# Kernel optimization log

Measured on AMD Instinct MI355X. Metric: run time of the kernel, lower is better.

The kernel has to match this reference:

```python
import jax, jax.numpy as jnp
import numpy as np

NUM_HEADS = 16
ROPE_THETA = 10000.0


def apply_rope(x, positions):
    # x: [B, H, S, D], positions: [S] int
    d = x.shape[-1]
    inv_freq = ROPE_THETA ** (-jnp.arange(0, d, 2, dtype=jnp.float32) / d)  # [D/2]
    ang = positions.astype(jnp.float32)[:, None] * inv_freq[None, :]        # [S, D/2]
    cos, sin = jnp.cos(ang), jnp.sin(ang)                                   # [S, D/2]
    x1, x2 = x[..., 0::2], x[..., 1::2]                                     # even/odd pairs
    r1 = x1 * cos - x2 * sin
    r2 = x1 * sin + x2 * cos
    return jnp.stack([r1, r2], axis=-1).reshape(x.shape)


def setup_inputs() -> dict:
    key = jax.random.key(0)
    k1, k2, k3 = jax.random.split(key, 3)
    B, S, D = 2, 2048, 2048
    x = jax.random.normal(k1, (B, S, D), dtype=jnp.float32)
    token_positions = jnp.arange(S, dtype=jnp.int64)
    w_qkv = jax.random.normal(k2, (D, 3 * D), dtype=jnp.float32) * (D ** -0.5)
    w_o = jax.random.normal(k3, (D, D), dtype=jnp.float32) * (D ** -0.5)
    return {"x": x, "token_positions": token_positions, "w_qkv": w_qkv, "w_o": w_o}


def reference(x, token_positions, w_qkv, w_o):
    B, S, D = x.shape
    H = NUM_HEADS
    hd = D // H
    qkv = x @ w_qkv                                   # [B, S, 3D]
    qkv = qkv.reshape(B, S, 3, H, hd)                 # split '(r h d)'
    q = jnp.transpose(qkv[:, :, 0], (0, 2, 1, 3))     # [B, H, S, hd]
    k = jnp.transpose(qkv[:, :, 1], (0, 2, 1, 3))
    v = jnp.transpose(qkv[:, :, 2], (0, 2, 1, 3))
    q = apply_rope(q, token_positions)
    k = apply_rope(k, token_positions)
    scale = 1.0 / jnp.sqrt(jnp.float32(hd))
    scores = jnp.einsum('bhqd,bhkd->bhqk', q, k) * scale  # [B, H, S, S]
    causal = jnp.tril(jnp.ones((S, S), dtype=bool))
    scores = jnp.where(causal[None, None], scores, jnp.float32(-1e30))
    attn = jax.nn.softmax(scores, axis=-1)
    a = jnp.einsum('bhqk,bhkd->bhqd', attn, v)            # [B, H, S, hd]
    a = jnp.transpose(a, (0, 2, 1, 3)).reshape(B, S, D)   # merge heads, h-major
    return a @ w_o
```

## Files before the change

### kernel.cpp

```cpp
#include <hip/hip_runtime.h>

#define SEQ  2048
#define DIM  2048
#define NH   16
#define HD   128
#define TDIM 6144
#define TT   4096

typedef float  f32x4  __attribute__((ext_vector_type(4)));
typedef __bf16 bf16x8 __attribute__((ext_vector_type(8)));

__device__ __forceinline__ unsigned short f2b(float f){
  union { float f; unsigned int u; } x; x.f = f;
  unsigned int r = x.u + 0x7FFFu + ((x.u >> 16) & 1u);
  return (unsigned short)(r >> 16);
}
__device__ __forceinline__ float b2f(unsigned short b){
  union { unsigned int u; float f; } x; x.u = ((unsigned int)b) << 16;
  return x.f;
}
__device__ __forceinline__ void gl_lds16(const void* g, void* l){
  __builtin_amdgcn_global_load_lds((const __attribute__((address_space(1))) unsigned int*)g,
                                   (__attribute__((address_space(3))) unsigned int*)l, 16, 0, 0);
}

__global__ __launch_bounds__(256) void k_prep(const float* __restrict__ x,
                                              unsigned short* __restrict__ xb,
                                              float2* __restrict__ tab){
  int bid = blockIdx.x;
  if (bid < 8192){
    int i = bid * 256 + threadIdx.x;
    float4 v = ((const float4*)x)[i];
    ushort4 o; o.x = f2b(v.x); o.y = f2b(v.y); o.z = f2b(v.z); o.w = f2b(v.w);
    ((ushort4*)xb)[i] = o;
  } else {
    int i = (bid - 8192) * 256 + threadIdx.x;
    int s = i >> 6, f = i & 63;
    double inv = pow(10000.0, -2.0 * (double)f / 128.0);
    double a = (double)s * inv;
    tab[i] = make_float2((float)cos(a), (float)sin(a));
  }
}

__global__ __launch_bounds__(256) void k_tconvB(const float* __restrict__ w_qkv,
                                                unsigned short* __restrict__ wqkvT,
                                                const float* __restrict__ w_o,
                                                unsigned short* __restrict__ woT){
  const float* in; unsigned short* out; int C;
  if (blockIdx.z == 0){ in = w_qkv; out = wqkvT; C = TDIM; }
  else                { in = w_o;   out = woT;   C = DIM;  }
  int c0 = blockIdx.x * 32;
  if (c0 >= C) return;
  __shared__ float t[64][33];
  int r0 = blockIdx.y * 64;
  int tx = threadIdx.x & 31, ty = threadIdx.x >> 5;
  for (int i = 0; i < 8; i++)
    t[ty + i*8][tx] = in[(size_t)(r0 + ty + i*8) * C + c0 + tx];
  __syncthreads();
  for (int i = 0; i < 4; i++){
    int c = ty + i*8;
    ushort2 o2; o2.x = f2b(t[2*tx][c]); o2.y = f2b(t[2*tx+1][c]);
    *(ushort2*)&out[(size_t)(c0 + c) * DIM + r0 + 2*tx] = o2;
  }
}

__global__ __launch_bounds__(256) void k_tv(const unsigned short* __restrict__ qkv,
                                            unsigned short* __restrict__ vT){
  __shared__ unsigned short t[64][65];
  int bh = blockIdx.z; int b = bh >> 4, h = bh & 15;
  const unsigned short* V = qkv + (size_t)b * SEQ * TDIM + 2 * DIM + h * HD;
  unsigned short* o = vT + (size_t)bh * HD * SEQ;
  int s0 = blockIdx.x * 64, d0 = blockIdx.y * 64;
  int tx = threadIdx.x & 31, ty = threadIdx.x >> 5;
  for (int i = 0; i < 8; i++){
    unsigned int v = *(const unsigned int*)&V[(size_t)(s0 + ty + i*8) * TDIM + d0 + 2*tx];
    t[ty + i*8][2*tx]   = (unsigned short)(v & 0xffffu);
    t[ty + i*8][2*tx+1] = (unsigned short)(v >> 16);
  }
  __syncthreads();
  for (int i = 0; i < 8; i++){
    int d = ty + i*8;
    ushort2 o2; o2.x = t[2*tx][d]; o2.y = t[2*tx+1][d];
    *(ushort2*)&o[(size_t)(d0 + d) * SEQ + s0 + 2*tx] = o2;
  }
}

template<bool OUT_F32, bool ROPE>
__global__ __launch_bounds__(512, 2) void k_gemm2(const unsigned short* __restrict__ A,
                                                  const unsigned short* __restrict__ BT,
                                                  void* __restrict__ Cout,
                                                  int M, int N, int K,
                                                  const float2* __restrict__ tab){
  __shared__ unsigned short sA[2*2*8192];
  __shared__ unsigned short sB[2*2*8192];
  int tid = threadIdx.x;
  int w = tid >> 6, l = tid & 63;
  int lm = l & 15, lq = l >> 4;
  int wm = w >> 2, wn = w & 3;
  int m0 = blockIdx.y * 256, n0 = blockIdx.x * 256;
  int NT = K >> 6;

  auto stA = [&](int buf, int half, int u){
    unsigned short* dst = sA + (buf*2 + half) * 8192;
    int grow0 = m0 + half*128;
#pragma unroll
    for (int j2 = 0; j2 < 2; j2++){
      int g = j2*512 + tid;
      int r = g >> 3, gc = g & 7;
      gl_lds16(A + (size_t)(grow0 + r) * K + u*64 + ((gc ^ (r & 7)) * 8), dst + g*8);
    }
  };
  auto stB = [&](int buf, int half, int u){
    unsigned short* dst = sB + (buf*2 + half) * 8192;
    int grow0 = n0 + half*128;
#pragma unroll
    for (int j2 = 0; j2 < 2; j2++){
      int g = j2*512 + tid;
      int r = g >> 3, gc = g & 7;
      gl_lds16(BT + (size_t)(grow0 + r) * K + u*64 + ((gc ^ (r & 7)) * 8), dst + g*8);
    }
  };

  f32x4 acc[2][2][4][2] = {};

  stA(0, 0, 0); stB(0, 1, 0); stA(0, 1, 0); stB(0, 0, 0);
  stA(1, 0, 1); stB(1, 1, 1);
  asm volatile("s_waitcnt vmcnt(4)" ::: "memory");
  __builtin_amdgcn_s_barrier();

  for (int t = 0; t < NT; t++){
    int cur = t & 1, nb = cur ^ 1;
    const unsigned short* sAb = sA + cur * 16384;
    const unsigned short* sBb = sB + cur * 16384;
    bf16x8 a[4][2], b0[2][2], b1[2][2];

#pragma unroll
    for (int i = 0; i < 4; i++){
      int r = wm*64 + i*16 + lm;
#pragma unroll
      for (int s = 0; s < 2; s++)
        a[i][s] = *(const bf16x8*)&sAb[r*64 + (((s*4 + lq) ^ (r & 7)) * 8)];
    }
#pragma unroll
    for (int j = 0; j < 2; j++){
      int r = wn*32 + j*16 + lm;
#pragma unroll
      for (int s = 0; s < 2; s++)
        b0[j][s] = *(const bf16x8*)&sBb[r*64 + (((s*4 + lq) ^ (r & 7)) * 8)];
    }
    __builtin_amdgcn_sched_barrier(0);
#pragma unroll
    for (int j = 0; j < 2; j++){
      int r = wn*32 + j*16 + lm;
#pragma unroll
      for (int s = 0; s < 2; s++)
        b1[j][s] = *(const bf16x8*)&sBb[8192 + r*64 + (((s*4 + lq) ^ (r & 7)) * 8)];
    }
    if (t + 1 < NT) stA(nb, 1, t + 1);
    asm volatile("s_waitcnt lgkmcnt(4)" ::: "memory");
    __builtin_amdgcn_sched_barrier(0);
    __builtin_amdgcn_s_setprio(1);
#pragma unroll
    for (int s = 0; s < 2; s++)
#pragma unroll
      for (int i = 0; i < 4; i++)
#pragma unroll
        for (int j = 0; j < 2; j++)
          acc[0][0][i][j] = __builtin_amdgcn_mfma_f32_16x16x32_bf16(a[i][s], b0[j][s],
                                                                    acc[0][0][i][j], 0, 0, 0);
    __builtin_amdgcn_s_setprio(0);
    __builtin_amdgcn_s_barrier();

    if (t + 1 < NT) stB(nb, 0, t + 1);
    asm volatile("s_waitcnt lgkmcnt(0)" ::: "memory");
    __builtin_amdgcn_sched_barrier(0);
    __builtin_amdgcn_s_setprio(1);
#pragma unroll
    for (int s = 0; s < 2; s++)
#pragma unroll
      for (int i = 0; i < 4; i++)
#pragma unroll
        for (int j = 0; j < 2; j++)
          acc[0][1][i][j] = __builtin_amdgcn_mfma_f32_16x16x32_bf16(a[i][s], b1[j][s],
                                                                    acc[0][1][i][j], 0, 0, 0);
    __builtin_amdgcn_s_setprio(0);
    __builtin_amdgcn_sched_barrier(0);
#pragma unroll
    for (int i = 0; i < 4; i++){
      int r = wm*64 + i*16 + lm;
#pragma unroll
      for (int s = 0; s < 2; s++)
        a[i][s] = *(const bf16x8*)&sAb[8192 + r*64 + (((s*4 + lq) ^ (r & 7)) * 8)];
    }
    __builtin_amdgcn_s_barrier();

    if (t + 2 < NT) stA(cur, 0, t + 2);
    asm volatile("s_waitcnt lgkmcnt(0)" ::: "memory");
    __builtin_amdgcn_sched_barrier(0);
    __builtin_amdgcn_s_setprio(1);
#pragma unroll
    for (int s = 0; s < 2; s++)
#pragma unroll
      for (int i = 0; i < 4; i++)
#pragma unroll
        for (int j = 0; j < 2; j++)
          acc[1][1][i][j] = __builtin_amdgcn_mfma_f32_16x16x32_bf16(a[i][s], b1[j][s],
                                                                    acc[1][1][i][j], 0, 0, 0);
    __builtin_amdgcn_s_setprio(0);
    __builtin_amdgcn_s_barrier();

    if (t + 2 < NT) stB(cur, 1, t + 2);
    __builtin_amdgcn_s_setprio(1);
#pragma unroll
    for (int s = 0; s < 2; s++)
#pragma unroll
      for (int i = 0; i < 4; i++)
#pragma unroll
        for (int j = 0; j < 2; j++)
          acc[1][0][i][j] = __builtin_amdgcn_mfma_f32_16x16x32_bf16(a[i][s], b0[j][s],
                                                                    acc[1][0][i][j], 0, 0, 0);
    __builtin_amdgcn_s_setprio(0);
    if (t + 2 < NT) asm volatile("s_waitcnt vmcnt(4)" ::: "memory");
    else            asm volatile("s_waitcnt vmcnt(0)" ::: "memory");
    __builtin_amdgcn_s_barrier();
  }

#pragma unroll
  for (int qm = 0; qm < 2; qm++)
#pragma unroll
    for (int qn = 0; qn < 2; qn++)
#pragma unroll
      for (int i = 0; i < 4; i++)
#pragma unroll
        for (int j = 0; j < 2; j++)
#pragma unroll
          for (int r = 0; r < 4; r++){
            int row = m0 + qm*128 + wm*64 + i*16 + lq*4 + r;
            int col = n0 + qn*128 + wn*32 + j*16 + lm;
            float v = acc[qm][qn][i][j][r];
            if (ROPE && col < 2*DIM){
              float p = __shfl_xor(v, 1);
              int s_ = row & (SEQ - 1);
              int f  = (col & 127) >> 1;
              float2 cs = tab[s_ * 64 + f];
              float sc2 = (col < DIM) ? 0.08838834764831845f : 1.0f;
              v = (lm & 1) ? (p * cs.y + v * cs.x) * sc2
                           : (v * cs.x - p * cs.y) * sc2;
            }
            if (OUT_F32) ((float*)Cout)[(size_t)row * N + col] = v;
            else ((unsigned short*)Cout)[(size_t)row * N + col] = f2b(v);
          }
}

__global__ __launch_bounds__(512, 2) void k_gemm3(const unsigned short* __restrict__ A,
                                                  const unsigned short* __restrict__ BT,
                                                  float* __restrict__ Cout,
                                                  int M, int N, int K){
  __shared__ unsigned short sA[2*2*8192];
  __shared__ unsigned short sB[2*8192];
  int tid = threadIdx.x;
  int w = tid >> 6, l = tid & 63;
  int lm = l & 15, lq = l >> 4;
  int wm = w >> 2, wn = w & 3;
  int m0 = blockIdx.y * 256, n0 = blockIdx.x * 128;
  int NT = K >> 6;

  auto stA = [&](int buf, int half, int u){
    unsigned short* dst = sA + (buf*2 + half) * 8192;
    int grow0 = m0 + half*128;
#pragma unroll
    for (int j2 = 0; j2 < 2; j2++){
      int g = j2*512 + tid;
      int r = g >> 3, gc = g & 7;
      gl_lds16(A + (size_t)(grow0 + r) * K + u*64 + ((gc ^ (r & 7)) * 8), dst + g*8);
    }
  };
  auto stB = [&](int buf, int u){
    unsigned short* dst = sB + buf * 8192;
#pragma unroll
    for (int j2 = 0; j2 < 2; j2++){
      int g = j2*512 + tid;
      int r = g >> 3, gc = g & 7;
      gl_lds16(BT + (size_t)(n0 + r) * K + u*64 + ((gc ^ (r & 7)) * 8), dst + g*8);
    }
  };

  f32x4 acc[2][4][2] = {};

  stB(0, 0); stA(0, 0, 0); stA(0, 1, 0);
  asm volatile("s_waitcnt vmcnt(2)" ::: "memory");
  __builtin_amdgcn_s_barrier();

  for (int t = 0; t < NT; t++){
    int cur = t & 1, nb = cur ^ 1;
    const unsigned short* sAb = sA + cur * 16384;
    const unsigned short* sBb = sB + cur * 8192;
    bf16x8 a[4][2], b[2][2];

#pragma unroll
    for (int i = 0; i < 4; i++){
      int r = wm*64 + i*16 + lm;
#pragma unroll
      for (int s = 0; s < 2; s++)
        a[i][s] = *(const bf16x8*)&sAb[r*64 + (((s*4 + lq) ^ (r & 7)) * 8)];
    }
#pragma unroll
    for (int j = 0; j < 2; j++){
      int r = wn*32 + j*16 + lm;
#pragma unroll
      for (int s = 0; s < 2; s++)
        b[j][s] = *(const bf16x8*)&sBb[r*64 + (((s*4 + lq) ^ (r & 7)) * 8)];
    }
    if (t + 1 < NT){ stB(nb, t + 1); stA(nb, 0, t + 1); }
    asm volatile("s_waitcnt lgkmcnt(0)" ::: "memory");
    __builtin_amdgcn_sched_barrier(0);
    __builtin_amdgcn_s_setprio(1);
#pragma unroll
    for (int s = 0; s < 2; s++)
#pragma unroll
      for (int i = 0; i < 4; i++)
#pragma unroll
        for (int j = 0; j < 2; j++)
          acc[0][i][j] = __builtin_amdgcn_mfma_f32_16x16x32_bf16(a[i][s], b[j][s],
                                                                 acc[0][i][j], 0, 0, 0);
    __builtin_amdgcn_s_setprio(0);
    if (t + 1 < NT) asm volatile("s_waitcnt vmcnt(4)" ::: "memory");
    else            asm volatile("s_waitcnt vmcnt(0)" ::: "memory");
    __builtin_amdgcn_s_barrier();

#pragma unroll
    for (int i = 0; i < 4; i++){
      int r = wm*64 + i*16 + lm;
#pragma unroll
      for (int s = 0; s < 2; s++)
        a[i][s] = *(const bf16x8*)&sAb[8192 + r*64 + (((s*4 + lq) ^ (r & 7)) * 8)];
    }
    if (t + 1 < NT) stA(nb, 1, t + 1);
    asm volatile("s_waitcnt lgkmcnt(0)" ::: "memory");
    __builtin_amdgcn_sched_barrier(0);
    __builtin_amdgcn_s_setprio(1);
#pragma unroll
    for (int s = 0; s < 2; s++)
#pragma unroll
      for (int i = 0; i < 4; i++)
#pragma unroll
        for (int j = 0; j < 2; j++)
          acc[1][i][j] = __builtin_amdgcn_mfma_f32_16x16x32_bf16(a[i][s], b[j][s],
                                                                 acc[1][i][j], 0, 0, 0);
    __builtin_amdgcn_s_setprio(0);
    if (t + 1 < NT) asm volatile("s_waitcnt vmcnt(2)" ::: "memory");
    else            asm volatile("s_waitcnt vmcnt(0)" ::: "memory");
    __builtin_amdgcn_s_barrier();
  }

#pragma unroll
  for (int qm = 0; qm < 2; qm++)
#pragma unroll
    for (int i = 0; i < 4; i++)
#pragma unroll
      for (int j = 0; j < 2; j++)
#pragma unroll
        for (int r = 0; r < 4; r++){
          int row = m0 + qm*128 + wm*64 + i*16 + lq*4 + r;
          int col = n0 + wn*32 + j*16 + lm;
          Cout[(size_t)row * N + col] = acc[qm][i][j][r];
        }
}

__global__ __launch_bounds__(256, 2) void k_flash(const unsigned short* __restrict__ qkv,
                                                  const unsigned short* __restrict__ vT,
                                                  unsigned short* __restrict__ ab){
  __shared__ unsigned short sK[2][64*128];
  __shared__ unsigned short sV[2][128*64];
  __shared__ unsigned short sP[4][16][68];
  int bh = blockIdx.x; int b = bh >> 4, h = bh & 15;
  int pr = blockIdx.y;
  int tid = threadIdx.x; int w = tid >> 6, l = tid & 63;
  int lm = l & 15, lq = l >> 4;
  const unsigned short* Q  = qkv + (size_t)b * SEQ * TDIM + h * HD;
  const unsigned short* Kp = Q + DIM;
  const unsigned short* Vh = vT + (size_t)bh * HD * SEQ;

  auto stageK = [&](unsigned short* dst, int k0){
    for (int p = 0; p < 4; p++){
      int r = w*16 + p*4 + (l >> 4);
      int g = (l & 15) ^ (r & 15);
      gl_lds16(Kp + (size_t)(k0 + r) * TDIM + g*8, dst + (w*16 + p*4)*128 + l*8);
    }
  };
  auto stageV = [&](unsigned short* dst, int k0){
    for (int p = 0; p < 4; p++){
      int r = w*32 + p*8 + (l >> 3);
      int g = (l & 7) ^ (r & 7);
      gl_lds16(Vh + (size_t)r * SEQ + k0 + g*8, dst + (w*32 + p*8)*64 + l*8);
    }
  };

  for (int seg = 0; seg < 2; seg++){
    int qt = seg ? (31 - pr) : pr;
    int q0 = qt * 64;
    int nkt = qt + 1;

    int qrow = q0 + w*16 + lm;
    bf16x8 qf[4];
    for (int ks = 0; ks < 4; ks++)
      qf[ks] = *(const bf16x8*)&Q[(size_t)qrow * TDIM + ks*32 + lq*8];

    f32x4 o[8] = {};
    float l_i[4] = {0.f, 0.f, 0.f, 0.f};

    stageK(sK[0], 0);
    stageV(sV[0], 0);
    __syncthreads();

    for (int kt = 0; kt < nkt; kt++){
      int cur = kt & 1;
      if (kt + 1 < nkt){
        stageK(sK[cur ^ 1], (kt+1) * 64);
        stageV(sV[cur ^ 1], (kt+1) * 64);
      }
      const unsigned short* sKb = sK[cur];
      const unsigned short* sVb = sV[cur];

      f32x4 sc[4] = {};
      for (int ks = 0; ks < 4; ks++)
        for (int nt = 0; nt < 4; nt++){
          bf16x8 kf = *(const bf16x8*)&sKb[(nt*16 + lm)*128 + (((ks*4 + lq) ^ lm) * 8)];
          sc[nt] = __builtin_amdgcn_mfma_f32_16x16x32_bf16(qf[ks], kf, sc[nt], 0, 0, 0);
        }

      int k0 = kt * 64;
      if (kt == qt){
        for (int nt = 0; nt < 4; nt++)
          for (int r = 0; r < 4; r++){
            float e = __expf(sc[nt][r]);
            if ((k0 + nt*16 + lm) > (q0 + w*16 + lq*4 + r)) e = 0.f;
            l_i[r] += e;
            sP[w][lq*4 + r][nt*16 + lm] = f2b(e);
          }
      } else {
        for (int nt = 0; nt < 4; nt++)
          for (int r = 0; r < 4; r++){
            float e = __expf(sc[nt][r]);
            l_i[r] += e;
            sP[w][lq*4 + r][nt*16 + lm] = f2b(e);
          }
      }

      for (int ks = 0; ks < 2; ks++){
        bf16x8 pf = *(const bf16x8*)&sP[w][lm][ks*32 + lq*8];
        for (int nt = 0; nt < 8; nt++){
          bf16x8 vf = *(const bf16x8*)&sVb[(nt*16 + lm)*64 + (((ks*4 + lq) ^ (lm & 7)) * 8)];
          o[nt] = __builtin_amdgcn_mfma_f32_16x16x32_bf16(pf, vf, o[nt], 0, 0, 0);
        }
      }

      __syncthreads();
    }

    for (int r = 0; r < 4; r++){
      float s = l_i[r];
      for (int d = 1; d < 16; d <<= 1) s += __shfl_xor(s, d, 16);
      float inv = 1.0f / s;
      int trow = b * SEQ + q0 + w*16 + lq*4 + r;
      for (int nt = 0; nt < 8; nt++)
        ab[(size_t)trow * DIM + h * HD + nt*16 + lm] = f2b(o[nt][r] * inv);
    }
  }
}

extern "C" void kernel_launch(void* const* d_in, const int* in_sizes, int n_in,
                              void* d_out, int out_size, void* d_ws, size_t ws_size,
                              hipStream_t stream){
  const float* x     = (const float*)d_in[0];
  const float* w_qkv = (const float*)d_in[2];
  const float* w_o   = (const float*)d_in[3];
  float* out = (float*)d_out;

  char* ws = (char*)d_ws;
  unsigned short* xb    = (unsigned short*)(ws);
  unsigned short* wqkvT = (unsigned short*)(ws + 16777216);
  unsigned short* woT   = (unsigned short*)(ws + 41943040);
  unsigned short* qkvb  = (unsigned short*)(ws + 50331648);
  unsigned short* vTb   = (unsigned short*)(ws + 100663296);
  unsigned short* abb   = (unsigned short*)(ws + 117440512);
  float2*         tab   = (float2*)(ws + 134217728);

  k_prep   <<<8704, 256, 0, stream>>>(x, xb, tab);
  k_tconvB <<<dim3(TDIM/32, DIM/64, 2), 256, 0, stream>>>(w_qkv, wqkvT, w_o, woT);
  k_gemm2<false,true><<<dim3(TDIM/256, TT/256), 512, 0, stream>>>(xb, wqkvT, qkvb,
                                                                  TT, TDIM, DIM, tab);
  k_tv     <<<dim3(SEQ/64, HD/64, 32), 256, 0, stream>>>(qkvb, vTb);
  k_flash  <<<dim3(32, 16), 256, 0, stream>>>(qkvb, vTb, abb);
  k_gemm3  <<<dim3(DIM/128, TT/256), 512, 0, stream>>>(abb, woT, out, TT, DIM, DIM);
}
```

Measured before the change: 400.9 us.

## Widen flash Q tile to 128 rows and split RoPE into a standalone kernel

The flash-attention kernel now gives each wave two 16-row Q groups, so a block covers 128 query rows and reuses each staged K/V tile for twice as many MFMAs. The grid is halved and launch bounds drop to one block per CU, so fewer waves are resident to hide latency. RoPE and the Q scaling move out of the QKV GEMM epilogue into a separate elementwise kernel. That removes the shuffle and table lookups from the GEMM store, but adds an extra read-write pass over the Q/K part of the bf16 qkv buffer. RoPE is also now applied to bf16-rounded values instead of the fp32 accumulators.

```diff
diff --git a/kernel.cpp b/kernel.cpp
--- a/kernel.cpp
+++ b/kernel.cpp
@@ -64,6 +64,27 @@
   }
 }
 
+__global__ __launch_bounds__(256) void k_rope(unsigned short* __restrict__ qkv,
+                                              const float2* __restrict__ tab){
+  int i = blockIdx.x * 256 + threadIdx.x;
+  int t   = i >> 11;
+  int rem = i & 2047;
+  int p   = rem >> 10;
+  int pi  = rem & 1023;
+  int h   = pi >> 6;
+  int f   = pi & 63;
+  int s   = t & (SEQ - 1);
+  size_t base = (size_t)t * TDIM + p * DIM + h * HD + f * 2;
+  unsigned int v = *(const unsigned int*)&qkv[base];
+  float x1 = b2f((unsigned short)(v & 0xffffu));
+  float x2 = b2f((unsigned short)(v >> 16));
+  float2 cs = tab[s * 64 + f];
+  float sc2 = (p == 0) ? 0.08838834764831845f : 1.0f;
+  float r1 = (x1 * cs.x - x2 * cs.y) * sc2;
+  float r2 = (x1 * cs.y + x2 * cs.x) * sc2;
+  *(unsigned int*)&qkv[base] = (unsigned int)f2b(r1) | ((unsigned int)f2b(r2) << 16);
+}
+
 __global__ __launch_bounds__(256) void k_tv(const unsigned short* __restrict__ qkv,
                                             unsigned short* __restrict__ vT){
   __shared__ unsigned short t[64][65];
@@ -85,12 +106,11 @@
   }
 }
 
-template<bool OUT_F32, bool ROPE>
+template<bool OUT_F32>
 __global__ __launch_bounds__(512, 2) void k_gemm2(const unsigned short* __restrict__ A,
                                                   const unsigned short* __restrict__ BT,
                                                   void* __restrict__ Cout,
-                                                  int M, int N, int K,
-                                                  const float2* __restrict__ tab){
+                                                  int M, int N, int K){
   __shared__ unsigned short sA[2*2*8192];
   __shared__ unsigned short sB[2*2*8192];
   int tid = threadIdx.x;
@@ -238,15 +258,6 @@
             int row = m0 + qm*128 + wm*64 + i*16 + lq*4 + r;
             int col = n0 + qn*128 + wn*32 + j*16 + lm;
             float v = acc[qm][qn][i][j][r];
-            if (ROPE && col < 2*DIM){
-              float p = __shfl_xor(v, 1);
-              int s_ = row & (SEQ - 1);
-              int f  = (col & 127) >> 1;
-              float2 cs = tab[s_ * 64 + f];
-              float sc2 = (col < DIM) ? 0.08838834764831845f : 1.0f;
-              v = (lm & 1) ? (p * cs.y + v * cs.x) * sc2
-                           : (v * cs.x - p * cs.y) * sc2;
-            }
             if (OUT_F32) ((float*)Cout)[(size_t)row * N + col] = v;
             else ((unsigned short*)Cout)[(size_t)row * N + col] = f2b(v);
           }
@@ -367,12 +378,12 @@
         }
 }
 
-__global__ __launch_bounds__(256, 2) void k_flash(const unsigned short* __restrict__ qkv,
+__global__ __launch_bounds__(256, 1) void k_flash(const unsigned short* __restrict__ qkv,
                                                   const unsigned short* __restrict__ vT,
                                                   unsigned short* __restrict__ ab){
   __shared__ unsigned short sK[2][64*128];
   __shared__ unsigned short sV[2][128*64];
-  __shared__ unsigned short sP[4][16][68];
+  __shared__ unsigned short sP[8][16][68];
   int bh = blockIdx.x; int b = bh >> 4, h = bh & 15;
   int pr = blockIdx.y;
   int tid = threadIdx.x; int w = tid >> 6, l = tid & 63;
@@ -382,6 +393,7 @@
   const unsigned short* Vh = vT + (size_t)bh * HD * SEQ;
 
   auto stageK = [&](unsigned short* dst, int k0){
+#pragma unroll
     for (int p = 0; p < 4; p++){
       int r = w*16 + p*4 + (l >> 4);
       int g = (l & 15) ^ (r & 15);
@@ -389,6 +401,7 @@
     }
   };
   auto stageV = [&](unsigned short* dst, int k0){
+#pragma unroll
     for (int p = 0; p < 4; p++){
       int r = w*32 + p*8 + (l >> 3);
       int g = (l & 7) ^ (r & 7);
@@ -397,17 +410,19 @@
   };
 
   for (int seg = 0; seg < 2; seg++){
-    int qt = seg ? (31 - pr) : pr;
-    int q0 = qt * 64;
-    int nkt = qt + 1;
-
-    int qrow = q0 + w*16 + lm;
-    bf16x8 qf[4];
-    for (int ks = 0; ks < 4; ks++)
-      qf[ks] = *(const bf16x8*)&Q[(size_t)qrow * TDIM + ks*32 + lq*8];
-
-    f32x4 o[8] = {};
-    float l_i[4] = {0.f, 0.f, 0.f, 0.f};
+    int qt = seg ? (15 - pr) : pr;
+    int q0 = qt * 128;
+    int nkt = 2*qt + 2;
+
+    bf16x8 qf[2][4];
+#pragma unroll
+    for (int rg = 0; rg < 2; rg++)
+#pragma unroll
+      for (int ks = 0; ks < 4; ks++)
+        qf[rg][ks] = *(const bf16x8*)&Q[(size_t)(q0 + w*32 + rg*16 + lm) * TDIM + ks*32 + lq*8];
+
+    f32x4 o[2][8] = {};
+    float l_i[2][4] = {};
 
     stageK(sK[0], 0);
     stageV(sV[0], 0);
@@ -422,50 +437,69 @@
       const unsigned short* sKb = sK[cur];
       const unsigned short* sVb = sV[cur];
 
-      f32x4 sc[4] = {};
+      f32x4 sc[2][4] = {};
+#pragma unroll
       for (int ks = 0; ks < 4; ks++)
+#pragma unroll
         for (int nt = 0; nt < 4; nt++){
           bf16x8 kf = *(const bf16x8*)&sKb[(nt*16 + lm)*128 + (((ks*4 + lq) ^ lm) * 8)];
-          sc[nt] = __builtin_amdgcn_mfma_f32_16x16x32_bf16(qf[ks], kf, sc[nt], 0, 0, 0);
+          sc[0][nt] = __builtin_amdgcn_mfma_f32_16x16x32_bf16(qf[0][ks], kf, sc[0][nt], 0, 0, 0);
+          sc[1][nt] = __builtin_amdgcn_mfma_f32_16x16x32_bf16(qf[1][ks], kf, sc[1][nt], 0, 0, 0);
         }
 
       int k0 = kt * 64;
-      if (kt == qt){
-        for (int nt = 0; nt < 4; nt++)
-          for (int r = 0; r < 4; r++){
-            float e = __expf(sc[nt][r]);
-            if ((k0 + nt*16 + lm) > (q0 + w*16 + lq*4 + r)) e = 0.f;
-            l_i[r] += e;
-            sP[w][lq*4 + r][nt*16 + lm] = f2b(e);
-          }
+      if (kt >= 2*qt){
+#pragma unroll
+        for (int rg = 0; rg < 2; rg++)
+#pragma unroll
+          for (int nt = 0; nt < 4; nt++)
+#pragma unroll
+            for (int r = 0; r < 4; r++){
+              float e = __expf(sc[rg][nt][r]);
+              if ((k0 + nt*16 + lm) > (q0 + w*32 + rg*16 + lq*4 + r)) e = 0.f;
+              l_i[rg][r] += e;
+              sP[w*2+rg][lq*4 + r][nt*16 + lm] = f2b(e);
+            }
       } else {
-        for (int nt = 0; nt < 4; nt++)
-          for (int r = 0; r < 4; r++){
-            float e = __expf(sc[nt][r]);
-            l_i[r] += e;
-            sP[w][lq*4 + r][nt*16 + lm] = f2b(e);
-          }
+#pragma unroll
+        for (int rg = 0; rg < 2; rg++)
+#pragma unroll
+          for (int nt = 0; nt < 4; nt++)
+#pragma unroll
+            for (int r = 0; r < 4; r++){
+              float e = __expf(sc[rg][nt][r]);
+              l_i[rg][r] += e;
+              sP[w*2+rg][lq*4 + r][nt*16 + lm] = f2b(e);
+            }
       }
 
+#pragma unroll
       for (int ks = 0; ks < 2; ks++){
-        bf16x8 pf = *(const bf16x8*)&sP[w][lm][ks*32 + lq*8];
+        bf16x8 pf0 = *(const bf16x8*)&sP[w*2+0][lm][ks*32 + lq*8];
+        bf16x8 pf1 = *(const bf16x8*)&sP[w*2+1][lm][ks*32 + lq*8];
+#pragma unroll
         for (int nt = 0; nt < 8; nt++){
           bf16x8 vf = *(const bf16x8*)&sVb[(nt*16 + lm)*64 + (((ks*4 + lq) ^ (lm & 7)) * 8)];
-          o[nt] = __builtin_amdgcn_mfma_f32_16x16x32_bf16(pf, vf, o[nt], 0, 0, 0);
+          o[0][nt] = __builtin_amdgcn_mfma_f32_16x16x32_bf16(pf0, vf, o[0][nt], 0, 0, 0);
+          o[1][nt] = __builtin_amdgcn_mfma_f32_16x16x32_bf16(pf1, vf, o[1][nt], 0, 0, 0);
         }
       }
 
       __syncthreads();
     }
 
-    for (int r = 0; r < 4; r++){
-      float s = l_i[r];
-      for (int d = 1; d < 16; d <<= 1) s += __shfl_xor(s, d, 16);
-      float inv = 1.0f / s;
-      int trow = b * SEQ + q0 + w*16 + lq*4 + r;
-      for (int nt = 0; nt < 8; nt++)
-        ab[(size_t)trow * DIM + h * HD + nt*16 + lm] = f2b(o[nt][r] * inv);
-    }
+#pragma unroll
+    for (int rg = 0; rg < 2; rg++)
+#pragma unroll
+      for (int r = 0; r < 4; r++){
+        float s = l_i[rg][r];
+        for (int d = 1; d < 16; d <<= 1) s += __shfl_xor(s, d, 16);
+        float inv = 1.0f / s;
+        int trow = b * SEQ + q0 + w*32 + rg*16 + lq*4 + r;
+#pragma unroll
+        for (int nt = 0; nt < 8; nt++)
+          ab[(size_t)trow * DIM + h * HD + nt*16 + lm] = f2b(o[rg][nt][r] * inv);
+      }
   }
 }
 
@@ -488,9 +522,9 @@
 
   k_prep   <<<8704, 256, 0, stream>>>(x, xb, tab);
   k_tconvB <<<dim3(TDIM/32, DIM/64, 2), 256, 0, stream>>>(w_qkv, wqkvT, w_o, woT);
-  k_gemm2<false,true><<<dim3(TDIM/256, TT/256), 512, 0, stream>>>(xb, wqkvT, qkvb,
-                                                                  TT, TDIM, DIM, tab);
+  k_gemm2<false><<<dim3(TDIM/256, TT/256), 512, 0, stream>>>(xb, wqkvT, qkvb, TT, TDIM, DIM);
+  k_rope   <<<TT * 2048 / 256, 256, 0, stream>>>(qkvb, tab);
   k_tv     <<<dim3(SEQ/64, HD/64, 32), 256, 0, stream>>>(qkvb, vTb);
-  k_flash  <<<dim3(32, 16), 256, 0, stream>>>(qkvb, vTb, abb);
+  k_flash  <<<dim3(32, 8), 256, 0, stream>>>(qkvb, vTb, abb);
   k_gemm3  <<<dim3(DIM/128, TT/256), 512, 0, stream>>>(abb, woT, out, TT, DIM, DIM);
 }
```

New measurement: 385.3 us. -3.9%, faster.
